# Kernel optimization log

Hardware: AMD Instinct MI355X
Metric: run time of the kernel (lower is better)

## Reference

```python
import jax, jax.numpy as jnp
import numpy as np

B_SZ, L_SEQ, D_DATA = 2, 1024, 8
D_CTRL = 256
POLY = 40
N_LAYERS = 2
D_STATE = 16
D_CONV = 4
D_INNER = 1 * D_CTRL          # expand_factor_control = 1
DT_RANK = -(-D_CTRL // 16)    # ceil(d_model/16) = 16
EPS = 1e-5


def setup_inputs() -> dict:
    key = jax.random.key(0)
    ks = jax.random.split(key, 12)
    s = 0.02
    x = jax.random.uniform(ks[0], (B_SZ, L_SEQ, D_DATA), dtype=jnp.float32)
    y = jax.random.uniform(ks[1], (B_SZ, L_SEQ, D_DATA), dtype=jnp.float32)
    return {
        'x': x,
        'y': y,
        # control_proj (note: fed 2*d_data features in structured forward)
        'control_proj_w': jax.random.normal(ks[2], (D_CTRL, 2 * D_DATA)) * s,
        'control_proj_b': jnp.zeros((D_CTRL,), jnp.float32),
        # stacked Mamba layer params (leading dim = n_layers)
        'norm_w': jnp.ones((N_LAYERS, D_CTRL), jnp.float32),
        'in_proj_w': jax.random.normal(ks[3], (N_LAYERS, 2 * D_INNER, D_CTRL)) * s,
        'conv_w': jax.random.normal(ks[4], (N_LAYERS, D_INNER, D_CONV)) * s,
        'conv_b': jnp.zeros((N_LAYERS, D_INNER), jnp.float32),
        'x_proj_w': jax.random.normal(ks[5], (N_LAYERS, DT_RANK + 2 * D_STATE, D_INNER)) * s,
        'dt_proj_w': jax.random.normal(ks[6], (N_LAYERS, D_INNER, DT_RANK)) * s,
        'dt_proj_b': jnp.zeros((N_LAYERS, D_INNER), jnp.float32),
        'A_log': jnp.tile(jnp.log(jnp.arange(1, D_STATE + 1, dtype=jnp.float32))[None, None, :], (N_LAYERS, D_INNER, 1)),
        'D_skip': jnp.ones((N_LAYERS, D_INNER), jnp.float32),
        'out_proj_w': jax.random.normal(ks[7], (N_LAYERS, D_CTRL, D_INNER)) * s,
        # b_net: Linear(d_control, 2*d_data*poly_dim^2)
        'b_net_w': jax.random.normal(ks[8], (2 * D_DATA * POLY * POLY, D_CTRL)) * s,
        'b_net_b': jnp.zeros((2 * D_DATA * POLY * POLY,), jnp.float32),
    }


def _rmsnorm(u, w):
    return u * jax.lax.rsqrt(jnp.mean(u * u, axis=-1, keepdims=True) + EPS) * w


def _causal_conv(u, w, b):
    # u: [B,L,C]; w: [C,K] depthwise causal conv, pad left K-1
    K = w.shape[-1]
    L = u.shape[1]
    up = jnp.pad(u, ((0, 0), (K - 1, 0), (0, 0)))
    acc = jnp.zeros_like(u)
    for k in range(K):  # K=4, fixed small kernel
        acc = acc + up[:, k:k + L, :] * w[:, k]
    return acc + b


def _mamba(u, norm_w, in_proj_w, conv_w, conv_b, x_proj_w, dt_proj_w, dt_proj_b, A_log, D_skip, out_proj_w):
    # mambapy-style stack of residual blocks: u = mixer(rmsnorm(u)) + u
    for i in range(N_LAYERS):
        r = _rmsnorm(u, norm_w[i])
        xz = jnp.einsum('bld,ed->ble', r, in_proj_w[i])          # [B,L,2*di]
        xc, zg = jnp.split(xz, 2, axis=-1)
        xc = jax.nn.silu(_causal_conv(xc, conv_w[i], conv_b[i]))  # [B,L,di]
        dbc = jnp.einsum('bld,ed->ble', xc, x_proj_w[i])          # [B,L,dt_rank+2*ds]
        delta = jax.nn.softplus(jnp.einsum('blr,dr->bld', dbc[..., :DT_RANK], dt_proj_w[i]) + dt_proj_b[i])
        Bm = dbc[..., DT_RANK:DT_RANK + D_STATE]
        Cm = dbc[..., DT_RANK + D_STATE:]
        A = -jnp.exp(A_log[i])                                    # [di,ds]
        dA = jnp.exp(delta[..., None] * A)                        # [B,L,di,ds]
        dBx = delta[..., None] * Bm[:, :, None, :] * xc[..., None]

        def step(h, inp):
            dA_t, dBx_t = inp
            h = dA_t * h + dBx_t
            return h, h

        h0 = jnp.zeros((u.shape[0], D_INNER, D_STATE), u.dtype)
        _, hs = jax.lax.scan(step, h0, (dA.transpose(1, 0, 2, 3), dBx.transpose(1, 0, 2, 3)))
        yv = jnp.einsum('lbds,lbs->bld', hs, Cm.transpose(1, 0, 2)) + D_skip[i] * xc
        yv = yv * jax.nn.silu(zg)
        u = jnp.einsum('bld,ed->ble', yv, out_proj_w[i]) + u
    return u


def _power_mat(z):
    # z ** arange(POLY), built with cumprod (grad-safe at exponent 0)
    ones = jnp.ones(z.shape + (1,), z.dtype)
    reps = jnp.broadcast_to(z[..., None], z.shape + (POLY - 1,))
    return jnp.cumprod(jnp.concatenate([ones, reps], axis=-1), axis=-1)  # [B,L,2d,P]


def reference(x, y, control_proj_w, control_proj_b, norm_w, in_proj_w, conv_w, conv_b,
              x_proj_w, dt_proj_w, dt_proj_b, A_log, D_skip, out_proj_w, b_net_w, b_net_b):
    B, L, d = x.shape
    xdot = y - x
    z = jnp.concatenate([x, xdot], axis=-1)                       # [B,L,2d]
    pm = _power_mat(z)                                            # [B,L,2d,P]
    ctrl_in = jnp.flip(jnp.concatenate([xdot, y], axis=-1), axis=1)
    ctrl_in = ctrl_in @ control_proj_w.T + control_proj_b
    sp = _mamba(ctrl_in, norm_w, in_proj_w, conv_w, conv_b, x_proj_w,
                dt_proj_w, dt_proj_b, A_log, D_skip, out_proj_w)
    state_pred = jnp.flip(sp, axis=1)                             # [B,L,d_ctrl]
    bmat = (state_pred @ b_net_w.T + b_net_b).reshape(B, L, 2 * d, POLY, POLY)
    pow1 = jnp.einsum('bldkj,bldk->bldj', bmat, pm)
    zdot = jnp.einsum('bldj,bldj->bld', pow1, jnp.flip(pm, axis=2))
    return zdot[:, 1:, :], state_pred
```

## Files before the change

kernel.cpp:

```cpp
#include <hip/hip_runtime.h>
#include <hip/hip_bf16.h>

#define B_SZ   2
#define LSEQ   1024
#define DD     8
#define DCTRL  256
#define POLY   40
#define NL     2
#define DSTATE 16
#define DCONV  4
#define DINNER 256
#define DTRANK 16
#define NBL    (B_SZ*LSEQ)
#define NROWS  (2*DD*POLY*POLY)
#define NSLOT  25
#define NCH    32
#define LCH    32

typedef __attribute__((ext_vector_type(8))) short bf16x8;
typedef __attribute__((ext_vector_type(8))) unsigned short us8;
typedef __attribute__((ext_vector_type(4))) unsigned short us4;
typedef __attribute__((ext_vector_type(4))) float f32x4;

__device__ __forceinline__ float sigmoidf_(float x){ return 1.f/(1.f+__expf(-x)); }
__device__ __forceinline__ float softplusf_(float x){ return fmaxf(x,0.f) + log1pf(__expf(-fabsf(x))); }
__device__ __forceinline__ unsigned short f2bf(float f){
  unsigned int u = __float_as_uint(f);
  unsigned int r = (u + 0x7fffu + ((u>>16)&1u)) >> 16;
  return (unsigned short)r;
}

__global__ void k_f2bf(const float* __restrict__ in, unsigned short* __restrict__ out, int n8){
  int i = blockIdx.x*blockDim.x + threadIdx.x;
  if (i>=n8) return;
  const float4* p = (const float4*)(in + (size_t)i*8);
  float4 a = p[0], b = p[1];
  us8 r;
  r[0]=f2bf(a.x); r[1]=f2bf(a.y); r[2]=f2bf(a.z); r[3]=f2bf(a.w);
  r[4]=f2bf(b.x); r[5]=f2bf(b.y); r[6]=f2bf(b.z); r[7]=f2bf(b.w);
  *(us8*)(out + (size_t)i*8) = r;
}

#define IPW_N8 (NL*512*256/8)
#define OPW_N8 (NL*256*256/8)
#define PRE_B0 ((IPW_N8+OPW_N8)/256)
#define PRE_B1 (NL*288*256/256)
#define PRE_B2 (16*NBL/256)
#define PRE_B3 (NBL*256/256)
#define PRE_B4 (NROWS*256/8/256)
__global__ void k_prologue(const float* __restrict__ ipw, const float* __restrict__ opw,
                           const float* __restrict__ dtw, const float* __restrict__ xpw,
                           const float* __restrict__ x,   const float* __restrict__ y,
                           const float* __restrict__ cpw, const float* __restrict__ cpb,
                           const float* __restrict__ bnw,
                           unsigned short* __restrict__ ipwb,
                           unsigned short* __restrict__ wcomb,
                           float* __restrict__ pmt, float* __restrict__ u,
                           unsigned short* __restrict__ Wb){
  int bx = blockIdx.x; int tid = threadIdx.x;
  if (bx < PRE_B0){
    int i = bx*256 + tid;
    const float* src = (i < IPW_N8) ? (ipw + (size_t)i*8) : (opw + (size_t)(i-IPW_N8)*8);
    const float4* p = (const float4*)src;
    float4 a = p[0], b = p[1];
    us8 r;
    r[0]=f2bf(a.x); r[1]=f2bf(a.y); r[2]=f2bf(a.z); r[3]=f2bf(a.w);
    r[4]=f2bf(b.x); r[5]=f2bf(b.y); r[6]=f2bf(b.z); r[7]=f2bf(b.w);
    *(us8*)(ipwb + (size_t)i*8) = r;
  } else if (bx < PRE_B0+PRE_B1){
    int idx = (bx-PRE_B0)*256 + tid;
    int e = idx & 255; int row = (idx>>8) % 288; int l = idx / (288*256);
    float v;
    if (row < 256){
      float s=0.f;
      #pragma unroll
      for (int r=0;r<16;++r) s += dtw[((size_t)l*256+row)*16+r] * xpw[((size_t)l*48+r)*256+e];
      v = s;
    } else {
      v = xpw[((size_t)l*48 + (row-240))*256 + e];
    }
    wcomb[idx] = f2bf(v);
  } else if (bx < PRE_B0+PRE_B1+PRE_B2){
    int idx = (bx-PRE_B0-PRE_B1)*256 + tid;
    int m = idx & (NBL-1); int c = idx >> 11;
    float z;
    if (c < 8) z = x[(size_t)m*8 + c];
    else       z = y[(size_t)m*8 + (c-8)] - x[(size_t)m*8 + (c-8)];
    float p = 1.f;
    #pragma unroll
    for (int j=0;j<POLY;++j){ pmt[((size_t)c*POLY+j)*NBL + m] = p; p*=z; }
  } else if (bx < PRE_B0+PRE_B1+PRE_B2+PRE_B3){
    int idx = (bx-PRE_B0-PRE_B1-PRE_B2)*256 + tid;
    int e = idx & 255; int m = idx >> 8;
    int bb = m >> 10; int lm = m & 1023; int lo = 1023 - lm;
    const float* xp = x + ((size_t)bb*1024+lo)*8;
    const float* yp = y + ((size_t)bb*1024+lo)*8;
    const float* wr = cpw + (size_t)e*16;
    float acc = cpb[e];
    #pragma unroll
    for (int d=0; d<8; ++d) acc += (yp[d]-xp[d])*wr[d];
    #pragma unroll
    for (int d=0; d<8; ++d) acc += yp[d]*wr[8+d];
    u[idx] = acc;
  } else {
    int i = (bx-PRE_B0-PRE_B1-PRE_B2-PRE_B3)*256 + tid;
    const float4* p = (const float4*)(bnw + (size_t)i*8);
    float4 a = p[0], b = p[1];
    us8 r;
    r[0]=f2bf(a.x); r[1]=f2bf(a.y); r[2]=f2bf(a.z); r[3]=f2bf(a.w);
    r[4]=f2bf(b.x); r[5]=f2bf(b.y); r[6]=f2bf(b.z); r[7]=f2bf(b.w);
    *(us8*)(Wb + (size_t)i*8) = r;
  }
}

__global__ void k_rms(const float* __restrict__ u, const float* __restrict__ nw,
                      unsigned short* __restrict__ rb){
  int m = blockIdx.x; int e = threadIdx.x;
  float v = u[(size_t)m*256 + e];
  float ss = v*v;
  #pragma unroll
  for (int off=32; off>0; off>>=1) ss += __shfl_down(ss, off);
  __shared__ float sred[4];
  __shared__ float srstd;
  int wid = e>>6; int lane = e&63;
  if (lane==0) sred[wid]=ss;
  __syncthreads();
  if (e==0){ float t = sred[0]+sred[1]+sred[2]+sred[3]; srstd = rsqrtf(t*(1.f/256.f) + 1e-5f); }
  __syncthreads();
  rb[(size_t)m*256+e] = f2bf(v * srstd * nw[e]);
}

__global__ void __launch_bounds__(256)
gemm_bf(const unsigned short* __restrict__ A, const unsigned short* __restrict__ B,
        int N, int K, const float* __restrict__ bias,
        float* __restrict__ C0, float* __restrict__ C1, int ldc, int mode){
  __shared__ __align__(16) unsigned short Asm[128*40];
  __shared__ __align__(16) unsigned short Bsm[64*40];
  int tid = threadIdx.x;
  int lane = tid & 63;
  int w = tid >> 6; int wr = w >> 1, wc = w & 1;
  int l15 = lane & 15, l4 = lane >> 4;
  int m0 = blockIdx.y*128, n0 = blockIdx.x*64;

  f32x4 acc[4][2];
  #pragma unroll
  for (int i=0;i<4;++i)
    #pragma unroll
    for (int j=0;j<2;++j){ acc[i][j][0]=0.f; acc[i][j][1]=0.f; acc[i][j][2]=0.f; acc[i][j][3]=0.f; }

  int nks = K >> 5;
  for (int ks=0; ks<nks; ++ks){
    int k0 = ks*32;
    #pragma unroll
    for (int g2=0; g2<2; ++g2){
      int g = tid + g2*256; int row = g>>2, c8 = g&3;
      *(us8*)&Asm[row*40 + c8*8] = *(const us8*)(A + (size_t)(m0+row)*K + k0 + c8*8);
    }
    {
      int row = tid>>2, c8 = tid&3; int bn = n0+row;
      us8 v;
      if (bn < N){
        v = *(const us8*)(B + (size_t)bn*K + k0 + c8*8);
      } else {
        for (int z=0;z<8;++z) v[z]=0;
      }
      *(us8*)&Bsm[row*40 + c8*8] = v;
    }
    __syncthreads();
    bf16x8 av[4], bv[2];
    #pragma unroll
    for (int i=0;i<4;++i) av[i] = *(bf16x8*)&Asm[(wr*64+i*16+l15)*40 + l4*8];
    #pragma unroll
    for (int j=0;j<2;++j) bv[j] = *(bf16x8*)&Bsm[(wc*32+j*16+l15)*40 + l4*8];
    #pragma unroll
    for (int i=0;i<4;++i)
      #pragma unroll
      for (int j=0;j<2;++j)
        acc[i][j] = __builtin_amdgcn_mfma_f32_16x16x32_bf16(av[i], bv[j], acc[i][j], 0,0,0);
    __syncthreads();
  }

  #pragma unroll
  for (int i=0;i<4;++i){
    #pragma unroll
    for (int j=0;j<2;++j){
      int n = n0 + wc*32 + j*16 + l15;
      #pragma unroll
      for (int q=0;q<4;++q){
        int m = m0 + wr*64 + i*16 + l4*4 + q;
        float v = acc[i][j][q];
        if (mode==0){
          C0[(size_t)m*ldc + n] = v;
        } else if (mode==1){
          C0[(size_t)m*ldc + n] += v;
        } else {
          if (n < 256) C0[(size_t)m*256 + n] = softplusf_(v + bias[n]);
          else if (n < N) C1[(size_t)m*32 + (n-256)] = v;
        }
      }
    }
  }
}

__global__ void k_convsilu(const float* __restrict__ xz, const float* __restrict__ cw,
                           const float* __restrict__ cb, float* __restrict__ xc,
                           unsigned short* __restrict__ xcb){
  int idx = blockIdx.x*blockDim.x + threadIdx.x;
  if (idx >= NBL*64) return;
  int d4 = (idx & 63) << 2; int m = idx >> 6;
  int bb = m>>10, l = m&1023;
  float4 w0 = *(const float4*)&cw[(d4+0)*4];
  float4 w1 = *(const float4*)&cw[(d4+1)*4];
  float4 w2 = *(const float4*)&cw[(d4+2)*4];
  float4 w3 = *(const float4*)&cw[(d4+3)*4];
  float4 cbv = *(const float4*)&cb[d4];
  float a0=cbv.x, a1=cbv.y, a2=cbv.z, a3=cbv.w;
  #pragma unroll
  for (int k=0;k<4;++k){
    int ls = l - 3 + k;
    if (ls >= 0){
      float4 v = *(const float4*)&xz[((size_t)(bb*1024+ls))*512 + d4];
      a0 += v.x * ((const float*)&w0)[k];
      a1 += v.y * ((const float*)&w1)[k];
      a2 += v.z * ((const float*)&w2)[k];
      a3 += v.w * ((const float*)&w3)[k];
    }
  }
  a0 = a0*sigmoidf_(a0); a1 = a1*sigmoidf_(a1);
  a2 = a2*sigmoidf_(a2); a3 = a3*sigmoidf_(a3);
  float4 o; o.x=a0; o.y=a1; o.z=a2; o.w=a3;
  *(float4*)&xc[(size_t)m*256 + d4] = o;
  us4 ob; ob[0]=f2bf(a0); ob[1]=f2bf(a1); ob[2]=f2bf(a2); ob[3]=f2bf(a3);
  *(us4*)&xcb[(size_t)m*256 + d4] = ob;
}

__global__ void k_scan1(const float* __restrict__ delta, const float* __restrict__ bc,
                        const float* __restrict__ xc, const float* __restrict__ alog,
                        float* __restrict__ hend, float* __restrict__ Pc){
  int blk = blockIdx.x;
  int dg = blk & 15; int ch = (blk>>4) & (NCH-1); int bb = blk >> 9;
  int tid = threadIdx.x; int dl = tid>>4; int s = tid&15; int d = dg*16+dl;
  float A = -__expf(alog[(size_t)d*16+s]);
  float h = 0.f, p = 1.f;
  size_t base = (size_t)bb*1024 + ch*LCH;
  #pragma unroll 4
  for (int t=0;t<LCH;++t){
    size_t mb = base + t;
    float de  = delta[mb*256+d];
    float Bv  = bc[mb*32+s];
    float xcv = xc[mb*256+d];
    float a = __expf(de*A);
    h = a*h + de*Bv*xcv;
    p *= a;
  }
  size_t o = (((size_t)bb*NCH+ch)*256+d)*16+s;
  hend[o]=h; Pc[o]=p;
}

__global__ void k_scan2(const float* __restrict__ hend, const float* __restrict__ Pc,
                        float* __restrict__ Hinit){
  int idx = blockIdx.x*blockDim.x + threadIdx.x;
  if (idx >= B_SZ*256*16) return;
  int bb = idx >> 12; int ds = idx & 4095;
  float H = 0.f;
  #pragma unroll
  for (int ch=0; ch<NCH; ++ch){
    size_t o = ((size_t)bb*NCH+ch)*4096 + ds;
    Hinit[o] = H;
    H = Pc[o]*H + hend[o];
  }
}

__global__ void k_scan3(const float* __restrict__ delta, const float* __restrict__ bc,
                        const float* __restrict__ xc, const float* __restrict__ xz,
                        const float* __restrict__ alog, const float* __restrict__ dskip,
                        const float* __restrict__ Hinit, unsigned short* __restrict__ yvb){
  int blk = blockIdx.x;
  int dg = blk & 15; int ch = (blk>>4) & (NCH-1); int bb = blk >> 9;
  int tid = threadIdx.x; int dl = tid>>4; int s = tid&15; int d = dg*16+dl;
  float A = -__expf(alog[(size_t)d*16+s]);
  float dsk = dskip[d];
  float h = Hinit[(((size_t)bb*NCH+ch)*256+d)*16+s];
  size_t base = (size_t)bb*1024 + ch*LCH;
  #pragma unroll 2
  for (int t=0;t<LCH;++t){
    size_t mb = base + t;
    float de  = delta[mb*256+d];
    float Bv  = bc[mb*32+s];
    float Cv  = bc[mb*32+16+s];
    float xcv = xc[mb*256+d];
    float a = __expf(de*A);
    h = a*h + de*Bv*xcv;
    float yval = h*Cv;
    yval += __shfl_xor(yval,1);
    yval += __shfl_xor(yval,2);
    yval += __shfl_xor(yval,4);
    yval += __shfl_xor(yval,8);
    if (s==0){
      float zg = xz[mb*512+256+d];
      yvb[mb*256+d] = f2bf((yval + dsk*xcv) * zg * sigmoidf_(zg));
    }
  }
}

__global__ void k_storesp(const float* __restrict__ u, float* __restrict__ outsp,
                          unsigned short* __restrict__ spb){
  int idx = blockIdx.x*blockDim.x+threadIdx.x;
  if (idx>=NBL*256) return;
  int e = idx & 255; int m = idx >> 8;
  int bb=m>>10, l=m&1023;
  float v = u[((size_t)(bb*1024 + (1023-l)))*256 + e];
  outsp[idx]=v; spb[idx]=f2bf(v);
}

__global__ void __launch_bounds__(512)
k_bnet_mfma(const unsigned short* __restrict__ spb, const unsigned short* __restrict__ Wb,
            const float* __restrict__ bnb, const float* __restrict__ pmt,
            float* __restrict__ part){
  __shared__ __align__(16) unsigned short Asm[2][256*40];
  __shared__ __align__(16) unsigned short Bsm[2][64*40];
  __shared__ float red[2][256];

  int tid = threadIdx.x;
  int lane = tid & 63;
  int w = tid >> 6;
  int wr = w >> 1, wc = w & 1;
  int l15 = lane & 15, l4 = lane >> 4;
  int bx = blockIdx.x;
  int m0 = blockIdx.y*256;
  int n0 = bx*64;

  int aRow0 = (tid)>>2,        aC0 = (tid)&3;
  int aRow1 = (tid+512)>>2,    aC1 = (tid+512)&3;
  int bRow  = tid>>2,          bC  = tid&3;
  const unsigned short* aSrc0 = spb + ((size_t)(m0+aRow0))*256 + aC0*8;
  const unsigned short* aSrc1 = spb + ((size_t)(m0+aRow1))*256 + aC1*8;
  const unsigned short* bSrc  = Wb  + ((size_t)(n0+bRow ))*256 + bC*8;

  f32x4 acc[4][2];
  #pragma unroll
  for (int i=0;i<4;++i)
    #pragma unroll
    for (int j=0;j<2;++j){ acc[i][j][0]=0.f; acc[i][j][1]=0.f; acc[i][j][2]=0.f; acc[i][j][3]=0.f; }

  us8 rA0 = *(const us8*)(aSrc0);
  us8 rA1 = *(const us8*)(aSrc1);
  us8 rB;
  if (tid < 256) rB = *(const us8*)(bSrc);
  *(us8*)&Asm[0][aRow0*40 + aC0*8] = rA0;
  *(us8*)&Asm[0][aRow1*40 + aC1*8] = rA1;
  if (tid < 256) *(us8*)&Bsm[0][bRow*40 + bC*8] = rB;
  __syncthreads();

  int cur = 0;
  for (int ks=0; ks<8; ++ks){
    if (ks < 7){
      int k0n = (ks+1)*32;
      rA0 = *(const us8*)(aSrc0 + k0n);
      rA1 = *(const us8*)(aSrc1 + k0n);
      if (tid < 256) rB = *(const us8*)(bSrc + k0n);
    }
    bf16x8 av[4], bv[2];
    #pragma unroll
    for (int i=0;i<4;++i) av[i] = *(bf16x8*)&Asm[cur][(wr*64+i*16+l15)*40 + l4*8];
    #pragma unroll
    for (int j=0;j<2;++j) bv[j] = *(bf16x8*)&Bsm[cur][(wc*32+j*16+l15)*40 + l4*8];
    #pragma unroll
    for (int i=0;i<4;++i)
      #pragma unroll
      for (int j=0;j<2;++j)
        acc[i][j] = __builtin_amdgcn_mfma_f32_16x16x32_bf16(av[i], bv[j], acc[i][j], 0,0,0);
    if (ks < 7){
      *(us8*)&Asm[cur^1][aRow0*40 + aC0*8] = rA0;
      *(us8*)&Asm[cur^1][aRow1*40 + aC1*8] = rA1;
      if (tid < 256) *(us8*)&Bsm[cur^1][bRow*40 + bC*8] = rB;
    }
    __syncthreads();
    cur ^= 1;
  }

  int c = bx/25, slot = bx%25;
  int rem0 = slot*64;
  float bnbv[2]; int kkv[2], jjv[2];
  #pragma unroll
  for (int j=0;j<2;++j){
    int nl = wc*32 + j*16 + l15;
    int rem = rem0 + nl;
    bnbv[j] = bnb[n0 + nl];
    kkv[j] = rem/40; jjv[j] = rem%40;
  }
  const float* pc  = pmt + (size_t)c*POLY*NBL;
  const float* pcf = pmt + (size_t)(15-c)*POLY*NBL;
  #pragma unroll
  for (int i=0;i<4;++i){
    int mb = m0 + wr*64 + i*16 + l4*4;
    f32x4 s; s[0]=0.f; s[1]=0.f; s[2]=0.f; s[3]=0.f;
    #pragma unroll
    for (int j=0;j<2;++j){
      f32x4 pk = *(const f32x4*)&pc [(size_t)kkv[j]*NBL + mb];
      f32x4 pj = *(const f32x4*)&pcf[(size_t)jjv[j]*NBL + mb];
      #pragma unroll
      for (int q=0;q<4;++q) s[q] += (acc[i][j][q] + bnbv[j]) * pk[q] * pj[q];
    }
    #pragma unroll
    for (int q=0;q<4;++q){
      float t = s[q];
      t += __shfl_xor(t,1); t += __shfl_xor(t,2);
      t += __shfl_xor(t,4); t += __shfl_xor(t,8);
      if (l15==0) red[wc][wr*64 + i*16 + l4*4 + q] = t;
    }
  }
  __syncthreads();
  if (tid < 256){
    float v = red[0][tid] + red[1][tid];
    part[((size_t)(c*NSLOT + slot))*NBL + m0 + tid] = v;
  }
}

__global__ void k_final(const float* __restrict__ part, float* __restrict__ out){
  int j = blockIdx.x*blockDim.x+threadIdx.x;
  if (j >= 16*2046) return;
  int c = j / 2046; int r = j % 2046;
  int bb = r / 1023; int l = r % 1023 + 1;
  size_t m = (size_t)bb*1024 + l;
  float s = 0.f;
  #pragma unroll
  for (int q=0;q<NSLOT;++q) s += part[((size_t)(c*NSLOT + q))*NBL + m];
  out[((size_t)(bb*1023 + (l-1)))*16 + c] = s;
}

extern "C" void kernel_launch(void* const* d_in, const int* in_sizes, int n_in,
                              void* d_out, int out_size, void* d_ws, size_t ws_size,
                              hipStream_t stream) {
  const float* x    = (const float*)d_in[0];
  const float* y    = (const float*)d_in[1];
  const float* cpw  = (const float*)d_in[2];
  const float* cpb  = (const float*)d_in[3];
  const float* nw   = (const float*)d_in[4];
  const float* ipw  = (const float*)d_in[5];
  const float* cvw  = (const float*)d_in[6];
  const float* cvb  = (const float*)d_in[7];
  const float* xpw  = (const float*)d_in[8];
  const float* dtw  = (const float*)d_in[9];
  const float* dtb  = (const float*)d_in[10];
  const float* alog = (const float*)d_in[11];
  const float* dsk  = (const float*)d_in[12];
  const float* opw  = (const float*)d_in[13];
  const float* bnw  = (const float*)d_in[14];
  const float* bnb  = (const float*)d_in[15];

  float* out      = (float*)d_out;
  float* out_zdot = out;
  float* out_sp   = out + 32736;

  float* ws = (float*)d_ws;
  size_t off = 0;
  float* u     = ws + off; off += (size_t)NBL*256;
  unsigned short* rb = (unsigned short*)(ws + off); off += (size_t)NBL*256/2;
  float* xz    = ws + off; off += (size_t)NBL*512;
  float* xc    = ws + off; off += (size_t)NBL*256;
  unsigned short* xcb = (unsigned short*)(ws + off); off += (size_t)NBL*256/2;
  float* delta = ws + off; off += (size_t)NBL*256;
  float* bcm   = ws + off; off += (size_t)NBL*32;
  unsigned short* yvb = (unsigned short*)(ws + off); off += (size_t)NBL*256/2;
  float* pmt   = ws + off; off += (size_t)NBL*16*POLY;
  float* part  = ws + off; off += (size_t)NSLOT*NBL*16;
  float* hend  = ws + off; off += (size_t)B_SZ*NCH*256*16;
  float* Pc    = ws + off; off += (size_t)B_SZ*NCH*256*16;
  float* Hinit = ws + off; off += (size_t)B_SZ*NCH*256*16;
  unsigned short* spb  = (unsigned short*)(ws + off); off += (size_t)NBL*256/2;
  unsigned short* ipwb = (unsigned short*)(ws + off); off += (size_t)(IPW_N8+OPW_N8)*4;
  unsigned short* wcomb= (unsigned short*)(ws + off); off += (size_t)NL*288*256/2;

  int wbEarly = ((off + (size_t)NROWS*256/2)*sizeof(float) <= ws_size) ? 1 : 0;
  unsigned short* Wb = wbEarly ? (unsigned short*)(ws + off) : (unsigned short*)ws;

  unsigned short* opwb = ipwb + (size_t)IPW_N8*8;

  int preBlocks = PRE_B0+PRE_B1+PRE_B2+PRE_B3 + (wbEarly ? PRE_B4 : 0);
  k_prologue<<<preBlocks, 256, 0, stream>>>(ipw, opw, dtw, xpw, x, y, cpw, cpb, bnw,
                                            ipwb, wcomb, pmt, u, Wb);

  for (int i=0;i<NL;++i){
    k_rms<<<NBL, 256, 0, stream>>>(u, nw + i*256, rb);
    gemm_bf<<<dim3(8,16), 256, 0, stream>>>(rb, ipwb + (size_t)i*512*256, 512, 256,
                                            nullptr, xz, nullptr, 512, 0);
    k_convsilu<<<(NBL*64+255)/256, 256, 0, stream>>>(xz, cvw + i*256*4, cvb + i*256, xc, xcb);
    gemm_bf<<<dim3(5,16), 256, 0, stream>>>(xcb, wcomb + (size_t)i*288*256, 288, 256,
                                            dtb + i*256, delta, bcm, 256, 2);
    k_scan1<<<B_SZ*NCH*16, 256, 0, stream>>>(delta, bcm, xc, alog + (size_t)i*256*16, hend, Pc);
    k_scan2<<<(B_SZ*256*16+255)/256, 256, 0, stream>>>(hend, Pc, Hinit);
    k_scan3<<<B_SZ*NCH*16, 256, 0, stream>>>(delta, bcm, xc, xz, alog + (size_t)i*256*16,
                                             dsk + i*256, Hinit, yvb);
    gemm_bf<<<dim3(4,16), 256, 0, stream>>>(yvb, opwb + (size_t)i*256*256, 256, 256,
                                            nullptr, u, nullptr, 256, 1);
  }

  k_storesp<<<(NBL*256+255)/256, 256, 0, stream>>>(u, out_sp, spb);
  if (!wbEarly){
    k_f2bf<<<(NROWS*256/8 + 255)/256, 256, 0, stream>>>(bnw, Wb, NROWS*256/8);
  }
  k_bnet_mfma<<<dim3(NROWS/64, NBL/256), 512, 0, stream>>>(spb, Wb, bnb, pmt, part);
  k_final<<<(16*2046+255)/256, 256, 0, stream>>>(part, out_zdot);
}
```

Before: 256.4 us.

## Fuse final residual store into out-proj GEMM, shrink GEMM tiles, prioritize MFMA

The small gemm_bf kernel moves from 128x64 to 64x64 tiles, doubling the grid so more blocks spread across CUs. A new epilogue mode in the last layer's out-projection adds the residual, writes the flipped state_pred in fp32 and bf16 directly, and removes the separate k_storesp kernel along with its extra read of u. The bnet kernel raises wave priority around its MFMA block with s_setprio. Smaller tiles cost more global loads per FLOP, and the fused epilogue does scattered stores to flipped rows.

```diff
diff --git a/kernel.cpp b/kernel.cpp
--- a/kernel.cpp
+++ b/kernel.cpp
@@ -133,31 +133,29 @@
 __global__ void __launch_bounds__(256)
 gemm_bf(const unsigned short* __restrict__ A, const unsigned short* __restrict__ B,
         int N, int K, const float* __restrict__ bias,
-        float* __restrict__ C0, float* __restrict__ C1, int ldc, int mode){
-  __shared__ __align__(16) unsigned short Asm[128*40];
+        float* __restrict__ C0, float* __restrict__ C1, int ldc, int mode,
+        float* __restrict__ outsp, unsigned short* __restrict__ spb){
+  __shared__ __align__(16) unsigned short Asm[64*40];
   __shared__ __align__(16) unsigned short Bsm[64*40];
   int tid = threadIdx.x;
   int lane = tid & 63;
   int w = tid >> 6; int wr = w >> 1, wc = w & 1;
   int l15 = lane & 15, l4 = lane >> 4;
-  int m0 = blockIdx.y*128, n0 = blockIdx.x*64;
-
-  f32x4 acc[4][2];
-  #pragma unroll
-  for (int i=0;i<4;++i)
+  int m0 = blockIdx.y*64, n0 = blockIdx.x*64;
+
+  f32x4 acc[2][2];
+  #pragma unroll
+  for (int i=0;i<2;++i)
     #pragma unroll
     for (int j=0;j<2;++j){ acc[i][j][0]=0.f; acc[i][j][1]=0.f; acc[i][j][2]=0.f; acc[i][j][3]=0.f; }
 
+  int row = tid>>2, c8 = tid&3;
   int nks = K >> 5;
   for (int ks=0; ks<nks; ++ks){
     int k0 = ks*32;
-    #pragma unroll
-    for (int g2=0; g2<2; ++g2){
-      int g = tid + g2*256; int row = g>>2, c8 = g&3;
-      *(us8*)&Asm[row*40 + c8*8] = *(const us8*)(A + (size_t)(m0+row)*K + k0 + c8*8);
-    }
+    *(us8*)&Asm[row*40 + c8*8] = *(const us8*)(A + (size_t)(m0+row)*K + k0 + c8*8);
     {
-      int row = tid>>2, c8 = tid&3; int bn = n0+row;
+      int bn = n0+row;
       us8 v;
       if (bn < N){
         v = *(const us8*)(B + (size_t)bn*K + k0 + c8*8);
@@ -167,13 +165,13 @@
       *(us8*)&Bsm[row*40 + c8*8] = v;
     }
     __syncthreads();
-    bf16x8 av[4], bv[2];
-    #pragma unroll
-    for (int i=0;i<4;++i) av[i] = *(bf16x8*)&Asm[(wr*64+i*16+l15)*40 + l4*8];
+    bf16x8 av[2], bv[2];
+    #pragma unroll
+    for (int i=0;i<2;++i) av[i] = *(bf16x8*)&Asm[(wr*32+i*16+l15)*40 + l4*8];
     #pragma unroll
     for (int j=0;j<2;++j) bv[j] = *(bf16x8*)&Bsm[(wc*32+j*16+l15)*40 + l4*8];
     #pragma unroll
-    for (int i=0;i<4;++i)
+    for (int i=0;i<2;++i)
       #pragma unroll
       for (int j=0;j<2;++j)
         acc[i][j] = __builtin_amdgcn_mfma_f32_16x16x32_bf16(av[i], bv[j], acc[i][j], 0,0,0);
@@ -181,21 +179,27 @@
   }
 
   #pragma unroll
-  for (int i=0;i<4;++i){
+  for (int i=0;i<2;++i){
     #pragma unroll
     for (int j=0;j<2;++j){
       int n = n0 + wc*32 + j*16 + l15;
       #pragma unroll
       for (int q=0;q<4;++q){
-        int m = m0 + wr*64 + i*16 + l4*4 + q;
+        int m = m0 + wr*32 + i*16 + l4*4 + q;
         float v = acc[i][j][q];
         if (mode==0){
           C0[(size_t)m*ldc + n] = v;
         } else if (mode==1){
           C0[(size_t)m*ldc + n] += v;
-        } else {
+        } else if (mode==2){
           if (n < 256) C0[(size_t)m*256 + n] = softplusf_(v + bias[n]);
           else if (n < N) C1[(size_t)m*32 + (n-256)] = v;
+        } else {
+          float t = C0[(size_t)m*ldc + n] + v;
+          int bb = m >> 10; int lq = m & 1023;
+          size_t mf = (size_t)bb*1024 + (1023-lq);
+          outsp[mf*256 + n] = t;
+          spb[mf*256 + n] = f2bf(t);
         }
       }
     }
@@ -303,16 +307,6 @@
   }
 }
 
-__global__ void k_storesp(const float* __restrict__ u, float* __restrict__ outsp,
-                          unsigned short* __restrict__ spb){
-  int idx = blockIdx.x*blockDim.x+threadIdx.x;
-  if (idx>=NBL*256) return;
-  int e = idx & 255; int m = idx >> 8;
-  int bb=m>>10, l=m&1023;
-  float v = u[((size_t)(bb*1024 + (1023-l)))*256 + e];
-  outsp[idx]=v; spb[idx]=f2bf(v);
-}
-
 __global__ void __launch_bounds__(512)
 k_bnet_mfma(const unsigned short* __restrict__ spb, const unsigned short* __restrict__ Wb,
             const float* __restrict__ bnb, const float* __restrict__ pmt,
@@ -365,11 +359,13 @@
     for (int i=0;i<4;++i) av[i] = *(bf16x8*)&Asm[cur][(wr*64+i*16+l15)*40 + l4*8];
     #pragma unroll
     for (int j=0;j<2;++j) bv[j] = *(bf16x8*)&Bsm[cur][(wc*32+j*16+l15)*40 + l4*8];
+    __builtin_amdgcn_s_setprio(1);
     #pragma unroll
     for (int i=0;i<4;++i)
       #pragma unroll
       for (int j=0;j<2;++j)
         acc[i][j] = __builtin_amdgcn_mfma_f32_16x16x32_bf16(av[i], bv[j], acc[i][j], 0,0,0);
+    __builtin_amdgcn_s_setprio(0);
     if (ks < 7){
       *(us8*)&Asm[cur^1][aRow0*40 + aC0*8] = rA0;
       *(us8*)&Asm[cur^1][aRow1*40 + aC1*8] = rA1;
@@ -483,20 +479,24 @@
 
   for (int i=0;i<NL;++i){
     k_rms<<<NBL, 256, 0, stream>>>(u, nw + i*256, rb);
-    gemm_bf<<<dim3(8,16), 256, 0, stream>>>(rb, ipwb + (size_t)i*512*256, 512, 256,
-                                            nullptr, xz, nullptr, 512, 0);
+    gemm_bf<<<dim3(8,32), 256, 0, stream>>>(rb, ipwb + (size_t)i*512*256, 512, 256,
+                                            nullptr, xz, nullptr, 512, 0, nullptr, nullptr);
     k_convsilu<<<(NBL*64+255)/256, 256, 0, stream>>>(xz, cvw + i*256*4, cvb + i*256, xc, xcb);
-    gemm_bf<<<dim3(5,16), 256, 0, stream>>>(xcb, wcomb + (size_t)i*288*256, 288, 256,
-                                            dtb + i*256, delta, bcm, 256, 2);
+    gemm_bf<<<dim3(5,32), 256, 0, stream>>>(xcb, wcomb + (size_t)i*288*256, 288, 256,
+                                            dtb + i*256, delta, bcm, 256, 2, nullptr, nullptr);
     k_scan1<<<B_SZ*NCH*16, 256, 0, stream>>>(delta, bcm, xc, alog + (size_t)i*256*16, hend, Pc);
     k_scan2<<<(B_SZ*256*16+255)/256, 256, 0, stream>>>(hend, Pc, Hinit);
     k_scan3<<<B_SZ*NCH*16, 256, 0, stream>>>(delta, bcm, xc, xz, alog + (size_t)i*256*16,
                                              dsk + i*256, Hinit, yvb);
-    gemm_bf<<<dim3(4,16), 256, 0, stream>>>(yvb, opwb + (size_t)i*256*256, 256, 256,
-                                            nullptr, u, nullptr, 256, 1);
-  }
-
-  k_storesp<<<(NBL*256+255)/256, 256, 0, stream>>>(u, out_sp, spb);
+    if (i < NL-1){
+      gemm_bf<<<dim3(4,32), 256, 0, stream>>>(yvb, opwb + (size_t)i*256*256, 256, 256,
+                                              nullptr, u, nullptr, 256, 1, nullptr, nullptr);
+    } else {
+      gemm_bf<<<dim3(4,32), 256, 0, stream>>>(yvb, opwb + (size_t)i*256*256, 256, 256,
+                                              nullptr, u, nullptr, 256, 3, out_sp, spb);
+    }
+  }
+
   if (!wbEarly){
     k_f2bf<<<(NROWS*256/8 + 255)/256, 256, 0, stream>>>(bnw, Wb, NROWS*256/8);
   }
```

Result: faster. 229.3 us (-10.6%).
